# Optimization experiments

Measured on AMD Instinct MI355X. Metric: run time of the kernel, lower is better.

The kernel has to match this reference:

```python
import jax, jax.numpy as jnp
import numpy as np

EPS_RMS = 1.1920929e-07  # torch.finfo(float32).eps, RMSNorm default when eps=None
EPS_BN = 1e-5            # BatchNorm1d default eps
NUM_CODES = 4096
EMBED_DIM = 64


def rms_norm(x):
    # nn.RMSNorm(embed_dim, elementwise_affine=False)
    ms = jnp.mean(x * x, axis=-1, keepdims=True)
    return x * jax.lax.rsqrt(ms + EPS_RMS)


def get_codebook(codebook_weight, bn_weight, bn_bias):
    # BatchNorm1d with track_running_stats=False: batch stats over codebook rows
    mean = jnp.mean(codebook_weight, axis=0)
    var = jnp.var(codebook_weight, axis=0)  # biased variance, as torch BN uses
    h = (codebook_weight - mean) * jax.lax.rsqrt(var + EPS_BN) * bn_weight + bn_bias
    return rms_norm(h)


def setup_inputs() -> dict:
    key = jax.random.key(0)
    k1, k2 = jax.random.split(key)
    z = jax.random.normal(k1, (8, 4096, EMBED_DIM), dtype=jnp.float32)
    # codebook init: uniform(-1/num_codes, 1/num_codes)
    codebook_weight = jax.random.uniform(
        k2, (NUM_CODES, EMBED_DIM), dtype=jnp.float32,
        minval=-1.0 / NUM_CODES, maxval=1.0 / NUM_CODES)
    bn_weight = jnp.ones((EMBED_DIM,), dtype=jnp.float32)
    bn_bias = jnp.zeros((EMBED_DIM,), dtype=jnp.float32)
    return {"z": z, "codebook_weight": codebook_weight,
            "bn_weight": bn_weight, "bn_bias": bn_bias}


def reference(z, codebook_weight, bn_weight, bn_bias):
    # c_in / c_out are Identity since width == embed_dim
    z_e = rms_norm(z)                                   # [B, S, D]
    cb = get_codebook(codebook_weight, bn_weight, bn_bias)  # [K, D]

    z_flat = z_e.reshape(-1, z_e.shape[-1])             # [N, D]
    # argmin of cdist == argmin of squared distance (sqrt is monotone)
    d2 = (jnp.sum(z_flat * z_flat, axis=1, keepdims=True)
          - 2.0 * (z_flat @ cb.T)
          + jnp.sum(cb * cb, axis=1))                   # [N, K]
    q = jnp.argmin(d2, axis=1)                          # [N]

    z_q = cb[q].reshape(z_e.shape)                      # gather codes
    q = q.reshape(z_e.shape[:-1])

    # straight-through: gradient flows to z_e only
    z_q_st = z_e + jax.lax.stop_gradient(z_q - z_e)
    # ret_dict entries: 'z' (detached z_e), 'q', 'z_q' (detached)
    return (z_q_st, jax.lax.stop_gradient(z_e), q, jax.lax.stop_gradient(z_q))
```

## Files before the change

kernel.cpp:

```cpp
#include <hip/hip_runtime.h>
#include <math.h>

#define NROWS 32768
#define DIM   64
#define NCODE 4096
#define EPS_RMS 1.1920929e-07f
#define EPS_BN  1e-5f

typedef _Float16 f16x8 __attribute__((ext_vector_type(8)));
typedef float    f32x4 __attribute__((ext_vector_type(4)));

#define WS_PS   0
#define WS_PQ   16384
#define WS_CC   32768
#define WS_CB32 49152
#define WS_CH   (49152 + 1048576)
#define WS_CL   (WS_CH + 524288)

#define OUT1 ((size_t)NROWS * DIM)
#define OUT2 ((size_t)2 * NROWS * DIM)
#define OUT3 (OUT2 + NROWS)

#define MFMA16(a, b, c) __builtin_amdgcn_mfma_f32_16x16x32_f16(a, b, c, 0, 0, 0)

__device__ __forceinline__ void async_copy16(void* lds, const void* g) {
    __builtin_amdgcn_global_load_lds(
        (const __attribute__((address_space(1))) unsigned int*)g,
        (__attribute__((address_space(3))) unsigned int*)lds, 16, 0, 0);
}

__global__ __launch_bounds__(256) void k_bn1(const float* __restrict__ w,
                                             char* __restrict__ wsb) {
    __shared__ float s1[4][64], s2[4][64];
    int lane = threadIdx.x & 63, v = threadIdx.x >> 6;
    long base = (long)blockIdx.x * 64 + v * 16;
    float s = 0.f, sq = 0.f;
    #pragma unroll
    for (int i = 0; i < 16; i++) {
        float x = w[(base + i) * DIM + lane];
        s += x; sq += x * x;
    }
    s1[v][lane] = s; s2[v][lane] = sq;
    __syncthreads();
    if (threadIdx.x < 64) {
        float ts = s1[0][lane] + s1[1][lane] + s1[2][lane] + s1[3][lane];
        float tq = s2[0][lane] + s2[1][lane] + s2[2][lane] + s2[3][lane];
        ((float*)(wsb + WS_PS))[blockIdx.x * 64 + lane] = ts;
        ((float*)(wsb + WS_PQ))[blockIdx.x * 64 + lane] = tq;
    }
}

__global__ __launch_bounds__(256) void k_cb(const float* __restrict__ w,
                                            const float* __restrict__ bnw,
                                            const float* __restrict__ bnb,
                                            char* __restrict__ wsb) {
    __shared__ float s1[4][64], s2[4][64], af[64], bf[64];
    int t = threadIdx.x, lane = t & 63, v = t >> 6;
    const float* ps = (const float*)(wsb + WS_PS);
    const float* pq = (const float*)(wsb + WS_PQ);
    float s = 0.f, sq = 0.f;
    #pragma unroll
    for (int b = 0; b < 16; b++) {
        s  += ps[(v * 16 + b) * 64 + lane];
        sq += pq[(v * 16 + b) * 64 + lane];
    }
    s1[v][lane] = s; s2[v][lane] = sq;
    __syncthreads();
    if (t < 64) {
        float ts = s1[0][lane] + s1[1][lane] + s1[2][lane] + s1[3][lane];
        float tq = s2[0][lane] + s2[1][lane] + s2[2][lane] + s2[3][lane];
        float mean = ts * (1.0f / NCODE);
        float var  = tq * (1.0f / NCODE) - mean * mean;
        float a = rsqrtf(var + EPS_BN) * bnw[lane];
        af[lane] = a;
        bf[lane] = bnb[lane] - mean * a;
    }
    __syncthreads();
    float a = af[lane], bb = bf[lane];
    float*     cb32 = (float*)(wsb + WS_CB32);
    _Float16*  chG  = (_Float16*)(wsb + WS_CH);
    _Float16*  clG  = (_Float16*)(wsb + WS_CL);
    float*     ccp  = (float*)(wsb + WS_CC);
    #pragma unroll
    for (int i = 0; i < 4; i++) {
        long row = (long)blockIdx.x * 16 + v * 4 + i;
        float x = w[row * DIM + lane];
        float h = fmaf(x, a, bb);
        float ss = h * h;
        #pragma unroll
        for (int m = 1; m < 64; m <<= 1) ss += __shfl_xor(ss, m);
        float rms = rsqrtf(ss * (1.0f / DIM) + EPS_RMS);
        float c = h * rms;
        cb32[row * DIM + lane] = c;
        _Float16 ch = (_Float16)c;
        chG[row * DIM + lane] = ch;
        clG[row * DIM + lane] = (_Float16)(c - (float)ch);
        float cs = c * c;
        #pragma unroll
        for (int m = 1; m < 64; m <<= 1) cs += __shfl_xor(cs, m);
        if (lane == 0) ccp[row] = -0.5f * cs;
    }
}

__global__ __launch_bounds__(256, 2) void k_main(const float* __restrict__ z,
                                                 const char* __restrict__ wsb,
                                                 float* __restrict__ out) {
    __shared__ __align__(16) unsigned char sm[65536];

    const int tid  = threadIdx.x;
    const int lane = tid & 63;
    const int w    = tid >> 6;
    const int wr   = w >> 1;
    const int wc   = w & 1;
    const int l15  = lane & 15;
    const int l4   = lane >> 4;
    const long rowbase = (long)blockIdx.x * 64;

    const _Float16* chG  = (const _Float16*)(wsb + WS_CH);
    const _Float16* clG  = (const _Float16*)(wsb + WS_CL);
    const float*    ccnG = (const float*)(wsb + WS_CC);
    const float*    cb32 = (const float*)(wsb + WS_CB32);

    const int B0    = w * 4096 + lane * 16;
    const int scode = B0 >> 7;
    const int ssp   = (B0 >> 4) & 7;
    const long gsw  = (long)scode * DIM + (long)((ssp ^ (scode & 7)) * 8);

    #pragma unroll
    for (int i = 0; i < 4; i++) {
        async_copy16(sm + B0 + i * 1024,         chG + gsw + i * 8 * DIM / 8 * 8);
    }
    #pragma unroll
    for (int i = 0; i < 4; i++) {
        async_copy16(sm + 16384 + B0 + i * 1024, clG + gsw + i * 8 * DIM / 8 * 8);
    }

    {
        int r = tid >> 2, seg = tid & 3;
        const float* zrow = z + (rowbase + r) * DIM + seg * 16;
        float vv[16];
        float ss = 0.f;
        #pragma unroll
        for (int i = 0; i < 16; i++) { vv[i] = zrow[i]; ss += vv[i] * vv[i]; }
        ss += __shfl_xor(ss, 1);
        ss += __shfl_xor(ss, 2);
        float rms = rsqrtf(ss * (1.0f / DIM) + EPS_RMS);
        float* oz = out + OUT1 + (rowbase + r) * DIM + seg * 16;
        __align__(16) _Float16 hb[16], lb[16];
        #pragma unroll
        for (int i = 0; i < 16; i++) {
            float x = vv[i] * rms;
            oz[i] = x;
            _Float16 h = (_Float16)x;
            hb[i] = h;
            lb[i] = (_Float16)(x - (float)h);
        }
        unsigned char* zhp = sm + 32768 + r * 128 + seg * 32;
        unsigned char* zlp = sm + 40960 + r * 128 + seg * 32;
        ((f16x8*)zhp)[0] = ((f16x8*)hb)[0];
        ((f16x8*)zhp)[1] = ((f16x8*)hb)[1];
        ((f16x8*)zlp)[0] = ((f16x8*)lb)[0];
        ((f16x8*)zlp)[1] = ((f16x8*)lb)[1];
    }
    __syncthreads();

    f16x8 ah[2][2], al[2][2];
    #pragma unroll
    for (int s = 0; s < 2; s++)
        #pragma unroll
        for (int c = 0; c < 2; c++) {
            int arow = wr * 32 + s * 16 + l15;
            ah[s][c] = *(const f16x8*)(sm + 32768 + arow * 128 + c * 64 + l4 * 16);
            al[s][c] = *(const f16x8*)(sm + 40960 + arow * 128 + c * 64 + l4 * 16);
        }
    __syncthreads();

    int boff[4][2];
    #pragma unroll
    for (int q = 0; q < 4; q++) {
        int coderow = wc * 64 + q * 16 + l15;
        #pragma unroll
        for (int c = 0; c < 2; c++)
            boff[q][c] = coderow * 128 + ((c * 64 + l4 * 16) ^ ((coderow & 7) << 4));
    }

    float ccv[4];
    #pragma unroll
    for (int q = 0; q < 4; q++)
        ccv[q] = ccnG[wc * 64 + q * 16 + l15];

    float bmax[2][4];
    int   bix[2][4];
    #pragma unroll
    for (int s = 0; s < 2; s++)
        #pragma unroll
        for (int r = 0; r < 4; r++) { bmax[s][r] = -3.4e38f; bix[s][r] = 0; }

    for (int p = 0; p < 32; ++p) {
        float ccn_nx[4];
        if (p + 1 < 32) {
            const float* cn = ccnG + (p + 1) * 128;
            #pragma unroll
            for (int q = 0; q < 4; q++)
                ccn_nx[q] = cn[wc * 64 + q * 16 + l15];
            unsigned char* nb = sm + ((p + 1) & 1) * 32768;
            const _Float16* gh = chG + (long)(p + 1) * 128 * DIM + gsw;
            const _Float16* gl = clG + (long)(p + 1) * 128 * DIM + gsw;
            #pragma unroll
            for (int i = 0; i < 4; i++)
                async_copy16(nb + B0 + i * 1024,         gh + i * 512);
            #pragma unroll
            for (int i = 0; i < 4; i++)
                async_copy16(nb + 16384 + B0 + i * 1024, gl + i * 512);
        }

        const unsigned char* chT = sm + (p & 1) * 32768;
        const unsigned char* clT = chT + 16384;

        #pragma unroll 2
        for (int q = 0; q < 4; q++) {
            f16x8 bh[2], bl[2];
            #pragma unroll
            for (int c = 0; c < 2; c++) {
                bh[c] = *(const f16x8*)(chT + boff[q][c]);
                bl[c] = *(const f16x8*)(clT + boff[q][c]);
            }
            int code = p * 128 + wc * 64 + q * 16 + l15;
            f32x4 ci = {ccv[q], ccv[q], ccv[q], ccv[q]};
            #pragma unroll
            for (int s = 0; s < 2; s++) {
                f32x4 a0 = MFMA16(ah[s][0], bh[0], ci);
                a0 = MFMA16(ah[s][0], bl[0], a0);
                a0 = MFMA16(al[s][0], bh[0], a0);
                f32x4 zz = {0.f, 0.f, 0.f, 0.f};
                f32x4 a1 = MFMA16(ah[s][1], bh[1], zz);
                a1 = MFMA16(ah[s][1], bl[1], a1);
                a1 = MFMA16(al[s][1], bh[1], a1);
                #pragma unroll
                for (int r = 0; r < 4; r++) {
                    float v = a0[r] + a1[r];
                    if (v > bmax[s][r]) { bmax[s][r] = v; bix[s][r] = code; }
                }
            }
        }
        __syncthreads();
        #pragma unroll
        for (int q = 0; q < 4; q++) ccv[q] = ccn_nx[q];
    }

    float* redd = (float*)sm;
    int*   redi = (int*)(sm + 512);
    int*   bidx = (int*)(sm + 1024);
    #pragma unroll
    for (int s = 0; s < 2; s++)
        #pragma unroll
        for (int r = 0; r < 4; r++) {
            float d = bmax[s][r];
            int   ix = bix[s][r];
            #pragma unroll
            for (int m = 1; m < 16; m <<= 1) {
                float od = __shfl_xor(d, m);
                int   oi = __shfl_xor(ix, m);
                if (od > d || (od == d && oi < ix)) { d = od; ix = oi; }
            }
            if (l15 == 0) {
                int rowloc = wr * 32 + s * 16 + l4 * 4 + r;
                redd[rowloc * 2 + wc] = d;
                redi[rowloc * 2 + wc] = ix;
            }
        }
    __syncthreads();
    if (tid < 64) {
        float d0 = redd[tid * 2 + 0], d1 = redd[tid * 2 + 1];
        int   i0 = redi[tid * 2 + 0], i1 = redi[tid * 2 + 1];
        int ix = (d1 > d0 || (d1 == d0 && i1 < i0)) ? i1 : i0;
        bidx[tid] = ix;
        out[OUT2 + rowbase + tid] = (float)ix;
    }
    __syncthreads();
    {
        int r = tid >> 2, seg = tid & 3;
        int ix = bidx[r];
        const float* src = cb32 + (long)ix * DIM + seg * 16;
        float* o0 = out + (rowbase + r) * DIM + seg * 16;
        float* o3 = out + OUT3 + (rowbase + r) * DIM + seg * 16;
        #pragma unroll
        for (int i = 0; i < 16; i++) { float t = src[i]; o0[i] = t; o3[i] = t; }
    }
}

extern "C" void kernel_launch(void* const* d_in, const int* in_sizes, int n_in,
                              void* d_out, int out_size, void* d_ws, size_t ws_size,
                              hipStream_t stream) {
    const float* z   = (const float*)d_in[0];
    const float* w   = (const float*)d_in[1];
    const float* bnw = (const float*)d_in[2];
    const float* bnb = (const float*)d_in[3];
    float* out = (float*)d_out;
    char*  wsb = (char*)d_ws;

    k_bn1 <<<64,  256, 0, stream>>>(w, wsb);
    k_cb  <<<256, 256, 0, stream>>>(w, bnw, bnb, wsb);
    k_main<<<512, 256, 0, stream>>>(z, wsb, out);
}
```

Before: 87.66 us.

## Double block size to 8 waves, split codes across 4 wave columns

Raises k_main from 256 to 512 threads per block. The 128-code tile is now split across four wave columns of 32 codes each instead of two of 64, and each thread copies and normalises half as much data. The six MFMAs per tile are chained into a single accumulator rather than two partial sums that were added afterwards, and the last pass is peeled so the loop needs no prefetch branch. The goal is more waves in flight to hide LDS and MFMA latency. The costs are a 4-way cross-wave reduction, a launch bound of (512,4) that caps registers per thread, and 64KB of LDS per block, which may limit how many blocks fit on one CU.

```diff
diff --git a/kernel.cpp b/kernel.cpp
--- a/kernel.cpp
+++ b/kernel.cpp
@@ -102,7 +102,7 @@
     }
 }
 
-__global__ __launch_bounds__(256, 2) void k_main(const float* __restrict__ z,
+__global__ __launch_bounds__(512, 4) void k_main(const float* __restrict__ z,
                                                  const char* __restrict__ wsb,
                                                  float* __restrict__ out) {
     __shared__ __align__(16) unsigned char sm[65536];
@@ -110,8 +110,8 @@
     const int tid  = threadIdx.x;
     const int lane = tid & 63;
     const int w    = tid >> 6;
-    const int wr   = w >> 1;
-    const int wc   = w & 1;
+    const int wr   = w >> 2;
+    const int wc   = w & 3;
     const int l15  = lane & 15;
     const int l4   = lane >> 4;
     const long rowbase = (long)blockIdx.x * 64;
@@ -121,46 +121,39 @@
     const float*    ccnG = (const float*)(wsb + WS_CC);
     const float*    cb32 = (const float*)(wsb + WS_CB32);
 
-    const int B0    = w * 4096 + lane * 16;
+    const int B0    = w * 2048 + lane * 16;
     const int scode = B0 >> 7;
     const int ssp   = (B0 >> 4) & 7;
     const long gsw  = (long)scode * DIM + (long)((ssp ^ (scode & 7)) * 8);
 
-    #pragma unroll
-    for (int i = 0; i < 4; i++) {
-        async_copy16(sm + B0 + i * 1024,         chG + gsw + i * 8 * DIM / 8 * 8);
-    }
-    #pragma unroll
-    for (int i = 0; i < 4; i++) {
-        async_copy16(sm + 16384 + B0 + i * 1024, clG + gsw + i * 8 * DIM / 8 * 8);
-    }
+    async_copy16(sm + w * 2048,                chG + gsw);
+    async_copy16(sm + w * 2048 + 1024,         chG + gsw + 512);
+    async_copy16(sm + 16384 + w * 2048,        clG + gsw);
+    async_copy16(sm + 16384 + w * 2048 + 1024, clG + gsw + 512);
 
     {
-        int r = tid >> 2, seg = tid & 3;
-        const float* zrow = z + (rowbase + r) * DIM + seg * 16;
-        float vv[16];
+        int r = tid >> 3, seg = tid & 7;
+        const float* zrow = z + (rowbase + r) * DIM + seg * 8;
+        float vv[8];
         float ss = 0.f;
         #pragma unroll
-        for (int i = 0; i < 16; i++) { vv[i] = zrow[i]; ss += vv[i] * vv[i]; }
+        for (int i = 0; i < 8; i++) { vv[i] = zrow[i]; ss += vv[i] * vv[i]; }
         ss += __shfl_xor(ss, 1);
         ss += __shfl_xor(ss, 2);
+        ss += __shfl_xor(ss, 4);
         float rms = rsqrtf(ss * (1.0f / DIM) + EPS_RMS);
-        float* oz = out + OUT1 + (rowbase + r) * DIM + seg * 16;
-        __align__(16) _Float16 hb[16], lb[16];
-        #pragma unroll
-        for (int i = 0; i < 16; i++) {
+        float* oz = out + OUT1 + (rowbase + r) * DIM + seg * 8;
+        __align__(16) _Float16 hb[8], lb[8];
+        #pragma unroll
+        for (int i = 0; i < 8; i++) {
             float x = vv[i] * rms;
             oz[i] = x;
             _Float16 h = (_Float16)x;
             hb[i] = h;
             lb[i] = (_Float16)(x - (float)h);
         }
-        unsigned char* zhp = sm + 32768 + r * 128 + seg * 32;
-        unsigned char* zlp = sm + 40960 + r * 128 + seg * 32;
-        ((f16x8*)zhp)[0] = ((f16x8*)hb)[0];
-        ((f16x8*)zhp)[1] = ((f16x8*)hb)[1];
-        ((f16x8*)zlp)[0] = ((f16x8*)lb)[0];
-        ((f16x8*)zlp)[1] = ((f16x8*)lb)[1];
+        *(f16x8*)(sm + 32768 + r * 128 + seg * 16) = *(f16x8*)hb;
+        *(f16x8*)(sm + 40960 + r * 128 + seg * 16) = *(f16x8*)lb;
     }
     __syncthreads();
 
@@ -175,19 +168,20 @@
         }
     __syncthreads();
 
-    int boff[4][2];
-    #pragma unroll
-    for (int q = 0; q < 4; q++) {
-        int coderow = wc * 64 + q * 16 + l15;
+    int boff[2][2];
+    #pragma unroll
+    for (int q = 0; q < 2; q++) {
+        int coderow = wc * 32 + q * 16 + l15;
         #pragma unroll
         for (int c = 0; c < 2; c++)
             boff[q][c] = coderow * 128 + ((c * 64 + l4 * 16) ^ ((coderow & 7) << 4));
     }
-
-    float ccv[4];
-    #pragma unroll
-    for (int q = 0; q < 4; q++)
-        ccv[q] = ccnG[wc * 64 + q * 16 + l15];
+    const int codeoff = wc * 32 + l15;
+
+    float ccv[2];
+    #pragma unroll
+    for (int q = 0; q < 2; q++)
+        ccv[q] = ccnG[codeoff + q * 16];
 
     float bmax[2][4];
     int   bix[2][4];
@@ -196,61 +190,61 @@
         #pragma unroll
         for (int r = 0; r < 4; r++) { bmax[s][r] = -3.4e38f; bix[s][r] = 0; }
 
-    for (int p = 0; p < 32; ++p) {
-        float ccn_nx[4];
-        if (p + 1 < 32) {
-            const float* cn = ccnG + (p + 1) * 128;
-            #pragma unroll
-            for (int q = 0; q < 4; q++)
-                ccn_nx[q] = cn[wc * 64 + q * 16 + l15];
+    #define COMPUTE_PASS(p)                                                        \
+    {                                                                              \
+        const unsigned char* chT = sm + ((p) & 1) * 32768;                         \
+        const unsigned char* clT = chT + 16384;                                    \
+        _Pragma("unroll")                                                          \
+        for (int q = 0; q < 2; q++) {                                              \
+            f16x8 bh[2], bl[2];                                                    \
+            _Pragma("unroll")                                                      \
+            for (int c = 0; c < 2; c++) {                                          \
+                bh[c] = *(const f16x8*)(chT + boff[q][c]);                         \
+                bl[c] = *(const f16x8*)(clT + boff[q][c]);                         \
+            }                                                                      \
+            int code = (p) * 128 + codeoff + q * 16;                               \
+            f32x4 acc = {ccv[q], ccv[q], ccv[q], ccv[q]};                          \
+            _Pragma("unroll")                                                      \
+            for (int s = 0; s < 2; s++) {                                          \
+                f32x4 a2 = (s == 0) ? acc : (f32x4){ccv[q], ccv[q], ccv[q], ccv[q]}; \
+                a2 = MFMA16(ah[s][0], bh[0], a2);                                  \
+                a2 = MFMA16(ah[s][1], bh[1], a2);                                  \
+                a2 = MFMA16(ah[s][0], bl[0], a2);                                  \
+                a2 = MFMA16(ah[s][1], bl[1], a2);                                  \
+                a2 = MFMA16(al[s][0], bh[0], a2);                                  \
+                a2 = MFMA16(al[s][1], bh[1], a2);                                  \
+                _Pragma("unroll")                                                  \
+                for (int r = 0; r < 4; r++) {                                      \
+                    if (a2[r] > bmax[s][r]) { bmax[s][r] = a2[r]; bix[s][r] = code; } \
+                }                                                                  \
+            }                                                                      \
+        }                                                                          \
+    }
+
+    for (int p = 0; p < 31; ++p) {
+        {
             unsigned char* nb = sm + ((p + 1) & 1) * 32768;
-            const _Float16* gh = chG + (long)(p + 1) * 128 * DIM + gsw;
-            const _Float16* gl = clG + (long)(p + 1) * 128 * DIM + gsw;
-            #pragma unroll
-            for (int i = 0; i < 4; i++)
-                async_copy16(nb + B0 + i * 1024,         gh + i * 512);
-            #pragma unroll
-            for (int i = 0; i < 4; i++)
-                async_copy16(nb + 16384 + B0 + i * 1024, gl + i * 512);
-        }
-
-        const unsigned char* chT = sm + (p & 1) * 32768;
-        const unsigned char* clT = chT + 16384;
-
-        #pragma unroll 2
-        for (int q = 0; q < 4; q++) {
-            f16x8 bh[2], bl[2];
-            #pragma unroll
-            for (int c = 0; c < 2; c++) {
-                bh[c] = *(const f16x8*)(chT + boff[q][c]);
-                bl[c] = *(const f16x8*)(clT + boff[q][c]);
-            }
-            int code = p * 128 + wc * 64 + q * 16 + l15;
-            f32x4 ci = {ccv[q], ccv[q], ccv[q], ccv[q]};
-            #pragma unroll
-            for (int s = 0; s < 2; s++) {
-                f32x4 a0 = MFMA16(ah[s][0], bh[0], ci);
-                a0 = MFMA16(ah[s][0], bl[0], a0);
-                a0 = MFMA16(al[s][0], bh[0], a0);
-                f32x4 zz = {0.f, 0.f, 0.f, 0.f};
-                f32x4 a1 = MFMA16(ah[s][1], bh[1], zz);
-                a1 = MFMA16(ah[s][1], bl[1], a1);
-                a1 = MFMA16(al[s][1], bh[1], a1);
-                #pragma unroll
-                for (int r = 0; r < 4; r++) {
-                    float v = a0[r] + a1[r];
-                    if (v > bmax[s][r]) { bmax[s][r] = v; bix[s][r] = code; }
-                }
-            }
-        }
+            const _Float16* gh = chG + (long)(p + 1) * (128 * DIM) + gsw;
+            const _Float16* gl = clG + (long)(p + 1) * (128 * DIM) + gsw;
+            async_copy16(nb + w * 2048,                gh);
+            async_copy16(nb + w * 2048 + 1024,         gh + 512);
+            async_copy16(nb + 16384 + w * 2048,        gl);
+            async_copy16(nb + 16384 + w * 2048 + 1024, gl + 512);
+        }
+        float ccn_nx0 = ccnG[(p + 1) * 128 + codeoff];
+        float ccn_nx1 = ccnG[(p + 1) * 128 + codeoff + 16];
+
+        COMPUTE_PASS(p);
+
         __syncthreads();
-        #pragma unroll
-        for (int q = 0; q < 4; q++) ccv[q] = ccn_nx[q];
-    }
+        ccv[0] = ccn_nx0;
+        ccv[1] = ccn_nx1;
+    }
+    COMPUTE_PASS(31);
 
     float* redd = (float*)sm;
-    int*   redi = (int*)(sm + 512);
-    int*   bidx = (int*)(sm + 1024);
+    int*   redi = (int*)(sm + 1024);
+    int*   bidx = (int*)(sm + 2048);
     #pragma unroll
     for (int s = 0; s < 2; s++)
         #pragma unroll
@@ -265,27 +259,32 @@
             }
             if (l15 == 0) {
                 int rowloc = wr * 32 + s * 16 + l4 * 4 + r;
-                redd[rowloc * 2 + wc] = d;
-                redi[rowloc * 2 + wc] = ix;
+                redd[rowloc * 4 + wc] = d;
+                redi[rowloc * 4 + wc] = ix;
             }
         }
     __syncthreads();
     if (tid < 64) {
-        float d0 = redd[tid * 2 + 0], d1 = redd[tid * 2 + 1];
-        int   i0 = redi[tid * 2 + 0], i1 = redi[tid * 2 + 1];
-        int ix = (d1 > d0 || (d1 == d0 && i1 < i0)) ? i1 : i0;
-        bidx[tid] = ix;
-        out[OUT2 + rowbase + tid] = (float)ix;
+        float bv = redd[tid * 4];
+        int   bi_ = redi[tid * 4];
+        #pragma unroll
+        for (int j = 1; j < 4; j++) {
+            float dj = redd[tid * 4 + j];
+            int   ij = redi[tid * 4 + j];
+            if (dj > bv || (dj == bv && ij < bi_)) { bv = dj; bi_ = ij; }
+        }
+        bidx[tid] = bi_;
+        out[OUT2 + rowbase + tid] = (float)bi_;
     }
     __syncthreads();
     {
-        int r = tid >> 2, seg = tid & 3;
+        int r = tid >> 3, seg = tid & 7;
         int ix = bidx[r];
-        const float* src = cb32 + (long)ix * DIM + seg * 16;
-        float* o0 = out + (rowbase + r) * DIM + seg * 16;
-        float* o3 = out + OUT3 + (rowbase + r) * DIM + seg * 16;
-        #pragma unroll
-        for (int i = 0; i < 16; i++) { float t = src[i]; o0[i] = t; o3[i] = t; }
+        const float* src = cb32 + (long)ix * DIM + seg * 8;
+        float* o0 = out + (rowbase + r) * DIM + seg * 8;
+        float* o3 = out + OUT3 + (rowbase + r) * DIM + seg * 8;
+        #pragma unroll
+        for (int i = 0; i < 8; i++) { float t = src[i]; o0[i] = t; o3[i] = t; }
     }
 }
 
@@ -301,5 +300,5 @@
 
     k_bn1 <<<64,  256, 0, stream>>>(w, wsb);
     k_cb  <<<256, 256, 0, stream>>>(w, bnw, bnb, wsb);
-    k_main<<<512, 256, 0, stream>>>(z, wsb, out);
-}
+    k_main<<<512, 512, 0, stream>>>(z, wsb, out);
+}
```

New measurement: 72.46 us. 17.3% less time.
